# Optimization experiments

Measured on AMD Instinct MI355X. Metric: run time of the kernel, lower is better.

## Reference

```python
import jax, jax.numpy as jnp
import numpy as np

B, N, V, C, H, W = 4, 2048, 4, 64, 32, 32
D, K, OUT, HEADS = 128, 64, 256, 4
IMG_W, IMG_H = W * 14.0, H * 14.0
EPS_NORM = 1e-12


def setup_inputs() -> dict:
    key = jax.random.key(0)
    ks = iter(jax.random.split(key, 64))
    nk = lambda: next(ks)
    rn = lambda shape, s=1.0: jax.random.normal(nk(), shape, jnp.float32) * s
    eye4 = jnp.broadcast_to(jnp.eye(4, dtype=jnp.float32), (B, V, 4, 4))
    Kbase = jnp.array([[400.0, 0.0, IMG_W / 2], [0.0, 400.0, IMG_H / 2], [0.0, 0.0, 1.0]], jnp.float32)
    inp = {
        'gaussians': rn((B, N, 14)),
        'visual_feats': rn((B * V, C, H, W)),
        'extrinsics': eye4 + rn((B, V, 4, 4), 0.1),
        'intrinsics': jnp.broadcast_to(Kbase, (B, V, 3, 3)) + rn((B, V, 3, 3), 0.5),
        'offsets': rn((B, N, 2), 0.05),
        'pg_w': rn((D, 14), 0.1), 'pg_b': jnp.zeros((D,)), 'pg_ln_g': jnp.ones((D,)), 'pg_ln_b': jnp.zeros((D,)),
        'pv_w': rn((D, C), 0.1), 'pv_b': jnp.zeros((D,)), 'pv_ln_g': jnp.ones((D,)), 'pv_ln_b': jnp.zeros((D,)),
        'attn_ipw': rn((2, 3 * D, D), 0.05), 'attn_ipb': jnp.zeros((2, 3 * D)),
        'attn_ow': rn((2, D, D), 0.05), 'attn_ob': jnp.zeros((2, D)),
        'dca_ln_g': jnp.ones((2, D)), 'dca_ln_b': jnp.zeros((2, D)),
        'gate_w': rn((D, 2 * D), 0.05), 'gate_b': jnp.zeros((D,)),
        'router_w1': rn((D, 2 * D), 0.05), 'router_b1': jnp.zeros((D,)),
        'router_ln_g': jnp.ones((D,)), 'router_ln_b': jnp.zeros((D,)),
        'router_w2': rn((3, D), 0.01), 'router_b2': jnp.array([-3.0, -3.0, 2.0], jnp.float32),
        'vlad_cent': jnp.clip(rn((3, K, D), 0.01), -2.0, 2.0),
        'vlad_cw': rn((3, K, D), 0.05), 'vlad_cb': jnp.zeros((3, K)),
        'bn_w': rn((3, OUT, K * D), 0.01), 'bn_b': jnp.zeros((3, OUT)),
        'bn_ln_g': jnp.ones((3, OUT)), 'bn_ln_b': jnp.zeros((3, OUT)),
    }
    return inp


def _ln(x, g, b, eps=1e-5):
    m = x.mean(-1, keepdims=True)
    v = ((x - m) ** 2).mean(-1, keepdims=True)
    return (x - m) * jax.lax.rsqrt(v + eps) * g + b


def _l2n(x, axis):
    return x / jnp.maximum(jnp.linalg.norm(x, axis=axis, keepdims=True), EPS_NORM)


def _bilinear(fm, grid):
    # fm: [BV,H,W,C]; grid: [BV,N,2] in [-1,1]; align_corners=False, zero padding
    x = (grid[..., 0] + 1.0) * 0.5 * W - 0.5
    y = (grid[..., 1] + 1.0) * 0.5 * H - 0.5
    x0, y0 = jnp.floor(x), jnp.floor(y)
    fmf = fm.reshape(fm.shape[0], H * W, C)
    out = jnp.zeros((fm.shape[0], grid.shape[1], C), jnp.float32)
    for xi in (x0, x0 + 1.0):
        for yi in (y0, y0 + 1.0):
            wgt = (1.0 - jnp.abs(x - xi)) * (1.0 - jnp.abs(y - yi))
            valid = (xi >= 0) & (xi < W) & (yi >= 0) & (yi < H)
            idx = (jnp.clip(yi, 0, H - 1) * W + jnp.clip(xi, 0, W - 1)).astype(jnp.int32)
            v = jnp.take_along_axis(fmf, idx[..., None], axis=1)
            out = out + v * (wgt * valid.astype(jnp.float32))[..., None]
    return out


def _mha(q, k, v, ipw, ipb, ow, ob):
    Wq, Wk, Wv = jnp.split(ipw, 3, axis=0)
    bq, bk, bv = jnp.split(ipb, 3)
    dh = D // HEADS
    sh = lambda x, Wt, b: (x @ Wt.T + b).reshape(x.shape[0], x.shape[1], HEADS, dh)
    qh, kh, vh = sh(q, Wq, bq), sh(k, Wk, bk), sh(v, Wv, bv)
    att = jax.nn.softmax(jnp.einsum('bqhd,bkhd->bhqk', qh, kh) * (1.0 / np.sqrt(dh)), axis=-1)
    o = jnp.einsum('bhqk,bkhd->bqhd', att, vh).reshape(q.shape[0], q.shape[1], D)
    return o @ ow.T + ob


def _netvlad(x, cent, cw, cb):
    xn = _l2n(x, 2)                                   # [B,N,D]
    a = jax.nn.softmax(xn @ cw.T + cb, axis=-1)       # [B,N,K]
    # sum_n a[bnk]*(x[bnd]-c[kd]) without materializing [B,N,K,D]
    vlad = jnp.einsum('bnk,bnd->bkd', a, xn) - a.sum(1)[..., None] * cent
    vlad = _l2n(vlad, 2).reshape(x.shape[0], -1)
    return _l2n(vlad, 1)


def reference(gaussians, visual_feats, extrinsics, intrinsics, offsets,
              pg_w, pg_b, pg_ln_g, pg_ln_b, pv_w, pv_b, pv_ln_g, pv_ln_b,
              attn_ipw, attn_ipb, attn_ow, attn_ob, dca_ln_g, dca_ln_b,
              gate_w, gate_b, router_w1, router_b1, router_ln_g, router_ln_b,
              router_w2, router_b2, vlad_cent, vlad_cw, vlad_cb,
              bn_w, bn_b, bn_ln_g, bn_ln_b):
    # ---- DynamicProjectionLayer (vectorized over views) ----
    ph = jnp.concatenate([gaussians[:, :, :3], jnp.ones((B, N, 1), jnp.float32)], axis=2)
    cam = jnp.einsum('bvij,bnj->bvni', extrinsics, ph)          # [B,V,N,4]
    p2h = jnp.einsum('bvij,bvnj->bvni', intrinsics, cam[..., :3])
    depth = jnp.maximum(p2h[..., 2:3], 1e-6)
    p2 = p2h[..., :2] / depth
    grid = 2.0 * p2 / jnp.array([IMG_W, IMG_H], jnp.float32) - 1.0 + offsets[:, None]
    fm = visual_feats.reshape(B, V, C, H, W).transpose(0, 1, 3, 4, 2).reshape(B * V, H, W, C)
    sampled = _bilinear(fm, grid.reshape(B * V, N, 2)).reshape(B, V, N, C)
    valid = ((depth[..., 0] > 0.1) & (grid[..., 0] >= -1) & (grid[..., 0] <= 1)
             & (grid[..., 1] >= -1) & (grid[..., 1] <= 1)).astype(jnp.float32)[..., None]
    vfeat = (sampled * valid).sum(1) / (valid.sum(1) + 1e-8)     # [B,N,C]
    # ---- GaussianEncoder ----
    g_emb = jax.nn.relu(_ln(gaussians @ pg_w.T + pg_b, pg_ln_g, pg_ln_b))
    v_emb = jax.nn.relu(_ln(vfeat @ pv_w.T + pv_b, pv_ln_g, pv_ln_b))
    f_g2v = _ln(g_emb + _mha(g_emb, v_emb, v_emb, attn_ipw[0], attn_ipb[0], attn_ow[0], attn_ob[0]),
                dca_ln_g[0], dca_ln_b[0])
    f_v2g = _ln(v_emb + _mha(v_emb, g_emb, g_emb, attn_ipw[1], attn_ipb[1], attn_ow[1], attn_ob[1]),
                dca_ln_g[1], dca_ln_b[1])
    gate = jax.nn.sigmoid(jnp.concatenate([f_g2v, f_v2g], -1) @ gate_w.T + gate_b)
    fused = f_g2v * gate + f_v2g * (1.0 - gate)
    ri = jnp.concatenate([g_emb.mean(1), v_emb.mean(1)], -1)
    rw = jax.nn.softmax(jax.nn.relu(_ln(ri @ router_w1.T + router_b1, router_ln_g, router_ln_b))
                        @ router_w2.T + router_b2, axis=-1)
    descs = []
    for i, feat in enumerate((g_emb, v_emb, fused)):
        d = _netvlad(feat, vlad_cent[i], vlad_cw[i], vlad_cb[i])
        d = _ln(d @ bn_w[i].T + bn_b[i], bn_ln_g[i], bn_ln_b[i])
        descs.append(_l2n(d, 1))
    final = rw[:, 0:1] * descs[0] + rw[:, 1:2] * descs[1] + rw[:, 2:3] * descs[2]
    return _l2n(final, 1), rw
```

## Files before the change

kernel.cpp:

```cpp
#include <hip/hip_runtime.h>
#include <math.h>

typedef float f32x4 __attribute__((ext_vector_type(4)));
typedef short s16x8 __attribute__((ext_vector_type(8)));

#define DEV static __device__ __forceinline__

DEV float wsum(float v){
  #pragma unroll
  for(int m=1;m<64;m<<=1) v += __shfl_xor(v,m);
  return v;
}
template<int NW>
DEV float bsum(float v, float* s){
  v = wsum(v);
  int w = threadIdx.x>>6;
  if((threadIdx.x&63)==0) s[w]=v;
  __syncthreads();
  float r = 0.f;
  #pragma unroll
  for(int i=0;i<NW;++i) r += s[i];
  __syncthreads();
  return r;
}
DEV float xexp2(float x){
#if __has_builtin(__builtin_amdgcn_exp2f)
  return __builtin_amdgcn_exp2f(x);
#else
  return exp2f(x);
#endif
}
DEV unsigned pkbf(float lo, float hi){
  unsigned r;
  asm("v_cvt_pk_bf16_f32 %0, %1, %2" : "=v"(r) : "v"(lo), "v"(hi));
  return r;
}
DEV unsigned short bf16c(float v){ return (unsigned short)(pkbf(v, 0.f) & 0xffffu); }
DEV float ubf_lo(unsigned u){ unsigned b=(u&0xffffu)<<16; return __builtin_bit_cast(float,b); }
DEV float ubf_hi(unsigned u){ unsigned b=(u>>16)<<16;    return __builtin_bit_cast(float,b); }
union FR { unsigned u[4]; s16x8 v; uint4 q; };

DEV f32x4 MF(s16x8 a, s16x8 b, f32x4 c){
  return __builtin_amdgcn_mfma_f32_16x16x32_bf16(a, b, c, 0,0,0);
}

DEV void gl_lds16(const void* g, void* l){
  __builtin_amdgcn_global_load_lds(
    (const __attribute__((address_space(1))) void*)g,
    (__attribute__((address_space(3))) void*)l, 16, 0, 0);
}

__global__ __launch_bounds__(256) void k_proj(const float* __restrict__ gs, const float* __restrict__ vf,
                       const float* __restrict__ E, const float* __restrict__ Kin,
                       const float* __restrict__ off, float* __restrict__ vfeat){
  int bn = blockIdx.x*4 + (threadIdx.x>>6); int b = bn>>11; int c = threadIdx.x&63;
  const float* g = gs + (size_t)bn*14;
  float px = g[0], py = g[1], pz = g[2];
  float ox = off[bn*2+0], oy = off[bn*2+1];
  float acc = 0.f, vsum = 0.f;
  for(int v=0; v<4; ++v){
    const float* e = E + ((b*4+v)*16);
    float cx = e[0]*px + e[1]*py + e[2]*pz + e[3];
    float cy = e[4]*px + e[5]*py + e[6]*pz + e[7];
    float cz = e[8]*px + e[9]*py + e[10]*pz + e[11];
    const float* kk = Kin + ((b*4+v)*9);
    float ux = kk[0]*cx + kk[1]*cy + kk[2]*cz;
    float uy = kk[3]*cx + kk[4]*cy + kk[5]*cz;
    float uz = kk[6]*cx + kk[7]*cy + kk[8]*cz;
    float dep = fmaxf(uz, 1e-6f);
    float gx = 2.f*(ux/dep)*(1.f/448.f) - 1.f + ox;
    float gy = 2.f*(uy/dep)*(1.f/448.f) - 1.f + oy;
    float valid = (uz > 0.1f && gx >= -1.f && gx <= 1.f && gy >= -1.f && gy <= 1.f) ? 1.f : 0.f;
    float x = (gx+1.f)*16.f - 0.5f;
    float y = (gy+1.f)*16.f - 0.5f;
    float x0 = floorf(x), y0 = floorf(y);
    const float* fbase = vf + (size_t)((b*4+v)*64 + c)*1024;
    float sv = 0.f;
    #pragma unroll
    for(int t=0;t<4;++t){
      float xi = x0 + (float)(t&1), yi = y0 + (float)(t>>1);
      float wgt = (1.f - fabsf(x-xi))*(1.f - fabsf(y-yi));
      bool vt = (xi>=0.f && xi<32.f && yi>=0.f && yi<32.f);
      int xc = (int)fminf(fmaxf(xi,0.f),31.f);
      int yc = (int)fminf(fmaxf(yi,0.f),31.f);
      float smp = fbase[yc*32+xc];
      sv += vt ? wgt*smp : 0.f;
    }
    acc += valid * sv;
    vsum += valid;
  }
  vfeat[(size_t)bn*64 + c] = acc / (vsum + 1e-8f);
}

__global__ void k_embed(const float* __restrict__ gs, const float* __restrict__ vfeat,
   const float* __restrict__ pg_w, const float* __restrict__ pg_b,
   const float* __restrict__ pg_g, const float* __restrict__ pg_bb,
   const float* __restrict__ pv_w, const float* __restrict__ pv_b,
   const float* __restrict__ pv_g, const float* __restrict__ pv_bb,
   float* __restrict__ gemb, float* __restrict__ vemb,
   unsigned short* __restrict__ gembb, unsigned short* __restrict__ vembb){
  __shared__ float xs[64]; __shared__ float gsr[14]; __shared__ float red[2];
  int row = blockIdx.x; int d = threadIdx.x;
  if(d<14) gsr[d] = gs[(size_t)row*14+d];
  if(d<64) xs[d] = vfeat[(size_t)row*64+d];
  __syncthreads();
  float a = pg_b[d];
  #pragma unroll
  for(int j=0;j<14;++j) a += gsr[j]*pg_w[d*14+j];
  float mu = bsum<2>(a, red)*(1.f/128.f);
  float df = a-mu;
  float var = bsum<2>(df*df, red)*(1.f/128.f);
  float y = fmaxf(df*rsqrtf(var+1e-5f)*pg_g[d] + pg_bb[d], 0.f);
  gemb[(size_t)row*128+d] = y;
  gembb[(size_t)row*128+d] = bf16c(y);
  float av = pv_b[d];
  #pragma unroll
  for(int j=0;j<64;++j) av += xs[j]*pv_w[d*64+j];
  mu = bsum<2>(av, red)*(1.f/128.f);
  df = av-mu;
  var = bsum<2>(df*df, red)*(1.f/128.f);
  y = fmaxf(df*rsqrtf(var+1e-5f)*pv_g[d] + pv_bb[d], 0.f);
  vemb[(size_t)row*128+d] = y;
  vembb[(size_t)row*128+d] = bf16c(y);
}

__global__ void k_wprep(const float* __restrict__ ipw, const float* __restrict__ ow,
                        const float* __restrict__ gw, const float* __restrict__ cw,
                        unsigned short* __restrict__ WB){
  int i = blockIdx.x*256 + threadIdx.x;
  if(i >= 188416) return;
  float v;
  if(i < 98304)       v = ipw[i];
  else if(i < 131072) v = ow[i-98304];
  else if(i < 163840) v = gw[i-131072];
  else                v = cw[i-163840];
  WB[i] = bf16c(v);
}

__global__ __launch_bounds__(256) void k_qkv(const unsigned short* __restrict__ GEb,
    const unsigned short* __restrict__ VEb, const unsigned short* __restrict__ WB,
    const float* __restrict__ ipb, unsigned* __restrict__ QKVu, float qsc){
  int mt = blockIdx.x, y = blockIdx.y;
  int m = y/6, j6 = y%6, kind = j6>>1, n0 = (j6&1)*64;
  const unsigned short* A = (kind==0) ? (m?VEb:GEb) : (m?GEb:VEb);
  const unsigned short* W = WB + m*49152 + kind*16384;
  const float* bias = ipb + m*384 + kind*128;
  unsigned* outb = QKVu + (size_t)m*1572864 + (size_t)kind*524288;
  float scale = (kind==0)? qsc : 1.f;
  int m0 = mt*64;
  int wid=threadIdx.x>>6, lane=threadIdx.x&63, lr=lane&15, lg=lane>>4;
  const unsigned short* ap = A + (size_t)(m0+wid*16+lr)*128 + lg*8;
  f32x4 acc[4] = {{0,0,0,0},{0,0,0,0},{0,0,0,0},{0,0,0,0}};
  #pragma unroll
  for(int ks=0; ks<128; ks+=32){
    FR af; af.v = *(const s16x8*)(ap + ks);
    #pragma unroll
    for(int nt=0; nt<4; ++nt){
      FR bf; bf.v = *(const s16x8*)(W + (size_t)(n0+nt*16+lr)*128 + ks + lg*8);
      acc[nt] = MF(af.v, bf.v, acc[nt]);
    }
  }
  __shared__ float xs[64][65];
  #pragma unroll
  for(int nt=0; nt<4; ++nt){
    float bv = bias[n0+nt*16+lr];
    #pragma unroll
    for(int r=0;r<4;++r) xs[wid*16+lg*4+r][nt*16+lr] = (acc[nt][r]+bv)*scale;
  }
  __syncthreads();
  if(kind<2){
    int i = threadIdx.x>>2, s = threadIdx.x&3;
    int gr = m0 + i, b = gr>>11, nn = gr&2047;
    int j0 = n0 + s*16, h = j0>>5, d0 = j0&31;
    unsigned w[8];
    #pragma unroll
    for(int p=0;p<8;++p) w[p] = pkbf(xs[i][s*16+2*p], xs[i][s*16+2*p+1]);
    unsigned* dst = outb + ((size_t)(b*4+h)*2048+nn)*16 + (d0>>1);
    uint4 u0; u0.x=w[0];u0.y=w[1];u0.z=w[2];u0.w=w[3];
    uint4 u1; u1.x=w[4];u1.y=w[5];u1.z=w[6];u1.w=w[7];
    *(uint4*)dst = u0; *(uint4*)(dst+4) = u1;
  } else {
    int c = threadIdx.x>>2, rs = threadIdx.x&3;
    int j = n0 + c, h = j>>5, d = j&31;
    int b = m0>>11, nn0 = m0&2047;
    unsigned w[8];
    #pragma unroll
    for(int p=0;p<8;++p) w[p] = pkbf(xs[rs*16+2*p][c], xs[rs*16+2*p+1][c]);
    unsigned* dst = outb + (size_t)(b*4+h)*32768 + (size_t)d*1024 + ((nn0+rs*16)>>1);
    uint4 u0; u0.x=w[0];u0.y=w[1];u0.z=w[2];u0.w=w[3];
    uint4 u1; u1.x=w[4];u1.y=w[5];u1.z=w[6];u1.w=w[7];
    *(uint4*)dst = u0; *(uint4*)(dst+4) = u1;
  }
}

__global__ __launch_bounds__(256) void k_flash(const unsigned short* __restrict__ QKV,
    unsigned* __restrict__ OPARTw, float* __restrict__ LSUM){
  int qt = blockIdx.x, h = blockIdx.y, z = blockIdx.z;
  int mb = z&7, split = z>>3;
  int m = mb>>2, b = mb&3;
  const unsigned short* base = QKV + (size_t)m*3145728;
  const unsigned short* qp = base + (size_t)(b*4+h)*65536;
  const unsigned short* kp = qp + 1048576;
  const unsigned short* vp = qp + 2097152;
  int tid=threadIdx.x, wid=tid>>6, lane=tid&63, lr=lane&15, lg=lane>>4;
  __shared__ unsigned short KT[2][2048];
  __shared__ unsigned short VT[2][2048];
  __shared__ unsigned Ps[4][16][33];
  int q0 = qt*64 + wid*16;
  int kbase = split*1024;
  FR qf; qf.v = *(const s16x8*)(qp + (size_t)(q0+lr)*32 + lg*8);
  const f32x4 zz = {0.f,0.f,0.f,0.f};
  f32x4 o0g = zz, o1g = zz;
  float lrun = 0.f;
  unsigned* prow = &Ps[wid][lr][0];
  int kr = wid*16 + (lane>>2);
  int kscol = (((lane&3)<<3) ^ (((lane>>3)&3)<<3));
  const unsigned short* ksrc0 = kp + (size_t)(kbase + kr)*32 + kscol;
  int vrow = wid*8 + (lane>>3);
  int vscol = 8*((lane&7) ^ (lane>>3));
  const unsigned short* vsrc0 = vp + (size_t)vrow*2048 + kbase + vscol;
  int kkey = ((lr>>1)&3)<<3;
  int ko = lr*32 + ((lg*8) ^ kkey);
  int sw = (lr&7)*8;
  int vo0 = lr*64 + ((lg*8) ^ sw);
  int vo2 = lr*64 + ((32+lg*8) ^ sw);
  gl_lds16(ksrc0, &KT[0][wid*512]);
  gl_lds16(vsrc0, &VT[0][wid*512]);
  __syncthreads();
  int buf = 0;
  for(int t=0; t<16; ++t){
    int tn = (t+1)&15;
    gl_lds16(ksrc0 + (size_t)tn*2048, &KT[buf^1][wid*512]);
    gl_lds16(vsrc0 + tn*64,           &VT[buf^1][wid*512]);
    const unsigned short* Ktb = &KT[buf][0];
    const unsigned short* Vtb = &VT[buf][0];
    FR k0,k1,k2,k3;
    k0.v = *(const s16x8*)(Ktb + ko);
    k1.v = *(const s16x8*)(Ktb +  512 + ko);
    k2.v = *(const s16x8*)(Ktb + 1024 + ko);
    k3.v = *(const s16x8*)(Ktb + 1536 + ko);
    f32x4 s0 = MF(k0.v, qf.v, zz);
    f32x4 s1 = MF(k1.v, qf.v, zz);
    f32x4 s2 = MF(k2.v, qf.v, zz);
    f32x4 s3 = MF(k3.v, qf.v, zz);
    float p0[4],p1[4],p2[4],p3[4]; float ps=0.f;
    #pragma unroll
    for(int r=0;r<4;++r){
      p0[r]=xexp2(s0[r]); p1[r]=xexp2(s1[r]);
      p2[r]=xexp2(s2[r]); p3[r]=xexp2(s3[r]);
      ps += p0[r]+p1[r]+p2[r]+p3[r];
    }
    lrun += ps;
    asm volatile("" ::: "memory");
    prow[   lg*2+0]=pkbf(p0[0],p0[1]); prow[   lg*2+1]=pkbf(p0[2],p0[3]);
    prow[ 8+lg*2+0]=pkbf(p1[0],p1[1]); prow[ 8+lg*2+1]=pkbf(p1[2],p1[3]);
    prow[16+lg*2+0]=pkbf(p2[0],p2[1]); prow[16+lg*2+1]=pkbf(p2[2],p2[3]);
    prow[24+lg*2+0]=pkbf(p3[0],p3[1]); prow[24+lg*2+1]=pkbf(p3[2],p3[3]);
    asm volatile("" ::: "memory");
    FR pf0, pf1;
    #pragma unroll
    for(int i=0;i<4;++i){ pf0.u[i]=prow[lg*4+i]; pf1.u[i]=prow[16+lg*4+i]; }
    FR v0,v1,v2,v3;
    v0.v = *(const s16x8*)(Vtb + vo0);
    v1.v = *(const s16x8*)(Vtb + 1024 + vo0);
    v2.v = *(const s16x8*)(Vtb + vo2);
    v3.v = *(const s16x8*)(Vtb + 1024 + vo2);
    o0g = MF(v0.v, pf0.v, o0g);
    o1g = MF(v1.v, pf0.v, o1g);
    o0g = MF(v2.v, pf1.v, o0g);
    o1g = MF(v3.v, pf1.v, o1g);
    __syncthreads();
    buf ^= 1;
  }
  lrun += __shfl_xor(lrun,16); lrun += __shfl_xor(lrun,32);
  unsigned w00=pkbf(o0g[0],o0g[1]), w01=pkbf(o0g[2],o0g[3]);
  unsigned w10=pkbf(o1g[0],o1g[1]), w11=pkbf(o1g[2],o1g[3]);
  unsigned* op = OPARTw + ((size_t)(split*2+m)*8192 + (size_t)(b*2048+q0+lr))*64 + h*16 + lg*2;
  op[0]=w00; op[1]=w01; op[8]=w10; op[9]=w11;
  if(lg==0) LSUM[((size_t)(split*2+m)*16 + b*4+h)*2048 + q0+lr] = lrun;
}

__global__ __launch_bounds__(256) void k_oproj(const unsigned* __restrict__ OPARTw,
    const float* __restrict__ LSUM,
    const unsigned short* __restrict__ WB, const float* __restrict__ ob,
    const float* __restrict__ GE, const float* __restrict__ VE,
    const float* __restrict__ dg, const float* __restrict__ db,
    float* __restrict__ CC, unsigned short* __restrict__ CCb){
  int mt = blockIdx.x, m = blockIdx.y;
  int m0 = mt*64;
  const unsigned short* W = WB + 98304 + m*16384;
  const float* bias = ob + m*128;
  const float* R = m ? VE : GE;
  const float* gamma = dg + m*128;
  const float* beta  = db + m*128;
  int wid=threadIdx.x>>6, lane=threadIdx.x&63, lr=lane&15, lg=lane>>4;
  int gr = m0 + wid*16 + lr;
  int b2 = gr>>11, nn = gr&2047;
  float invh[4];
  #pragma unroll
  for(int h=0;h<4;++h){
    float l0 = LSUM[((size_t)(m*16) + b2*4+h)*2048 + nn];
    float l1 = LSUM[((size_t)((2+m)*16) + b2*4+h)*2048 + nn];
    invh[h] = 1.f/(l0+l1);
  }
  const unsigned* a0 = OPARTw + ((size_t)m*8192 + gr)*64 + lg*4;
  const unsigned* a1 = OPARTw + ((size_t)(2+m)*8192 + gr)*64 + lg*4;
  f32x4 acc[8] = {};
  #pragma unroll
  for(int ks=0; ks<4; ++ks){
    uint4 u0 = *(const uint4*)(a0 + ks*16);
    uint4 u1 = *(const uint4*)(a1 + ks*16);
    float sc = invh[ks];
    FR af;
    af.u[0] = pkbf((ubf_lo(u0.x)+ubf_lo(u1.x))*sc, (ubf_hi(u0.x)+ubf_hi(u1.x))*sc);
    af.u[1] = pkbf((ubf_lo(u0.y)+ubf_lo(u1.y))*sc, (ubf_hi(u0.y)+ubf_hi(u1.y))*sc);
    af.u[2] = pkbf((ubf_lo(u0.z)+ubf_lo(u1.z))*sc, (ubf_hi(u0.z)+ubf_hi(u1.z))*sc);
    af.u[3] = pkbf((ubf_lo(u0.w)+ubf_lo(u1.w))*sc, (ubf_hi(u0.w)+ubf_hi(u1.w))*sc);
    #pragma unroll
    for(int nt=0; nt<8; ++nt){
      FR bf; bf.v = *(const s16x8*)(W + (size_t)(nt*16+lr)*128 + ks*32 + lg*8);
      acc[nt] = MF(af.v, bf.v, acc[nt]);
    }
  }
  __shared__ float xs[64][129];
  __shared__ float mus[64], rss[64];
  #pragma unroll
  for(int nt=0; nt<8; ++nt){
    float bv = bias[nt*16+lr];
    #pragma unroll
    for(int r=0;r<4;++r){
      int row = wid*16+lg*4+r;
      xs[row][nt*16+lr] = acc[nt][r] + bv + R[(size_t)(m0+row)*128 + nt*16+lr];
    }
  }
  __syncthreads();
  if(threadIdx.x < 64){
    int row = threadIdx.x;
    float s=0.f, s2=0.f;
    #pragma unroll 8
    for(int c=0;c<128;++c){ float x = xs[row][c]; s += x; s2 += x*x; }
    float mu = s*(1.f/128.f);
    float var = fmaxf(s2*(1.f/128.f) - mu*mu, 0.f);
    mus[row] = mu; rss[row] = rsqrtf(var + 1e-5f);
  }
  __syncthreads();
  int row = threadIdx.x>>2, cs = (threadIdx.x&3)*32;
  float mu = mus[row], rs = rss[row];
  size_t obase = (size_t)(m0+row)*256 + m*128;
  #pragma unroll 8
  for(int c=cs;c<cs+32;++c){
    float y = (xs[row][c]-mu)*rs*gamma[c] + beta[c];
    CC [obase + c] = y;
    CCb[obase + c] = bf16c(y);
  }
}

__global__ __launch_bounds__(256) void k_gatef(const unsigned short* __restrict__ CCb,
    const unsigned short* __restrict__ WB, const float* __restrict__ gate_b,
    const float* __restrict__ CC, float* __restrict__ FU){
  int mt = blockIdx.x, nh = blockIdx.y;
  int m0 = mt*64, c0 = nh*64;
  const unsigned short* W = WB + 131072;
  int wid=threadIdx.x>>6, lane=threadIdx.x&63, lr=lane&15, lg=lane>>4;
  const unsigned short* ap = CCb + (size_t)(m0+wid*16+lr)*256 + lg*8;
  f32x4 acc[4] = {};
  #pragma unroll
  for(int ks=0; ks<256; ks+=32){
    FR af; af.v = *(const s16x8*)(ap + ks);
    #pragma unroll
    for(int nt=0; nt<4; ++nt){
      FR bf; bf.v = *(const s16x8*)(W + (size_t)(c0+nt*16+lr)*256 + ks + lg*8);
      acc[nt] = MF(af.v, bf.v, acc[nt]);
    }
  }
  #pragma unroll
  for(int nt=0; nt<4; ++nt){
    int col = c0 + nt*16+lr;
    float bv = gate_b[col];
    #pragma unroll
    for(int r=0;r<4;++r){
      int row = m0 + wid*16+lg*4+r;
      float gv = 1.f/(1.f+__expf(-(acc[nt][r]+bv)));
      FU[(size_t)row*128 + col] = CC[(size_t)row*256 + col]*gv
                                + CC[(size_t)row*256 + 128 + col]*(1.f-gv);
    }
  }
}

__global__ __launch_bounds__(256) void k_rpart(const float* __restrict__ gemb, const float* __restrict__ vemb,
                        float* __restrict__ part){
  int blk = blockIdx.x;
  int b = blk>>7, ch = blk&127, t = threadIdx.x;
  const float* src = (t<128)? gemb : vemb;
  int d = t&127;
  float s=0.f;
  int n0 = ch*16;
  for(int n=0;n<16;++n) s += src[((size_t)(b*2048+n0+n))*128 + d];
  part[(size_t)blk*256 + t] = s;
}
__global__ void k_router(const float* __restrict__ part, const float* __restrict__ w1,
     const float* __restrict__ b1, const float* __restrict__ lg, const float* __restrict__ lb,
     const float* __restrict__ w2, const float* __restrict__ b2,
     float* __restrict__ rw, float* __restrict__ outrw){
  __shared__ float ri[256]; __shared__ float red[2];
  int b = blockIdx.x, t = threadIdx.x;
  for(int j=t; j<256; j+=128){
    float s=0.f;
    for(int c=0;c<128;++c) s += part[(size_t)(b*128+c)*256 + j];
    ri[j] = s*(1.f/2048.f);
  }
  __syncthreads();
  float a = b1[t];
  for(int j=0;j<256;++j) a += ri[j]*w1[t*256+j];
  float mu = bsum<2>(a,red)*(1.f/128.f);
  float df = a-mu;
  float var = bsum<2>(df*df,red)*(1.f/128.f);
  float hv = fmaxf(df*rsqrtf(var+1e-5f)*lg[t]+lb[t], 0.f);
  float l0 = bsum<2>(hv*w2[t],red);
  float l1 = bsum<2>(hv*w2[128+t],red);
  float l2 = bsum<2>(hv*w2[256+t],red);
  if(t==0){
    l0+=b2[0]; l1+=b2[1]; l2+=b2[2];
    float mx = fmaxf(l0,fmaxf(l1,l2));
    float e0=__expf(l0-mx), e1=__expf(l1-mx), e2=__expf(l2-mx);
    float s=e0+e1+e2;
    rw[b*3+0]=e0/s; rw[b*3+1]=e1/s; rw[b*3+2]=e2/s;
    outrw[b*3+0]=e0/s; outrw[b*3+1]=e1/s; outrw[b*3+2]=e2/s;
  }
}

__global__ __launch_bounds__(256) void k_vlad1(
      const float* __restrict__ GE, const float* __restrict__ VE, const float* __restrict__ FU,
      const unsigned short* __restrict__ WBcw, const float* __restrict__ cbp,
      float* __restrict__ p0, float* __restrict__ p1, float* __restrict__ p2,
      float* __restrict__ asump){
  int ch = blockIdx.x, b = blockIdx.y, z = blockIdx.z;
  const float* feat = (z==0)?GE:((z==1)?VE:FU);
  const unsigned short* cwb = WBcw + z*8192;
  const float* cb = cbp + z*64;
  float* part = (z==0)?p0:((z==1)?p1:p2);
  float* asu = asump + z*8192;
  int t = threadIdx.x;
  __shared__ unsigned xnbu[64*36];
  __shared__ unsigned short xnbT[128*72];
  __shared__ unsigned abTu[64*36];
  int nbase = b*2048 + ch*64;
  {
    int r = t>>2, q = t&3;
    const float* frow = feat + (size_t)(nbase + r)*128 + q*32;
    float v[32]; float ssq = 0.f;
    #pragma unroll
    for(int i=0;i<8;++i){
      float4 f4 = *(const float4*)(frow + i*4);
      v[i*4+0]=f4.x; v[i*4+1]=f4.y; v[i*4+2]=f4.z; v[i*4+3]=f4.w;
      ssq += f4.x*f4.x+f4.y*f4.y+f4.z*f4.z+f4.w*f4.w;
    }
    ssq += __shfl_xor(ssq,1); ssq += __shfl_xor(ssq,2);
    float inv = 1.f/fmaxf(sqrtf(ssq),1e-12f);
    #pragma unroll
    for(int i=0;i<16;++i)
      xnbu[r*36 + q*8 + i] = pkbf(v[2*i]*inv, v[2*i+1]*inv);
    #pragma unroll
    for(int j=0;j<32;++j)
      xnbT[(q*32+j)*72 + r] = bf16c(v[j]*inv);
  }
  __syncthreads();
  int w = t>>6, lane = t&63, lr = lane&15, lg = lane>>4;
  {
    f32x4 acc[4] = {};
    #pragma unroll
    for(int ks=0; ks<4; ++ks){
      FR af; af.q = *(const uint4*)&xnbu[(w*16+lr)*36 + ks*16 + lg*4];
      #pragma unroll
      for(int nt=0; nt<4; ++nt){
        FR bf; bf.v = *(const s16x8*)(cwb + (size_t)(nt*16+lr)*128 + ks*32 + lg*8);
        acc[nt] = MF(af.v, bf.v, acc[nt]);
      }
    }
    float p[4][4]; float srow[4] = {0.f,0.f,0.f,0.f};
    #pragma unroll
    for(int nt=0;nt<4;++nt){
      float cbv = cb[nt*16+lr];
      #pragma unroll
      for(int rr=0;rr<4;++rr){
        p[nt][rr] = __expf(acc[nt][rr] + cbv);
        srow[rr] += p[nt][rr];
      }
    }
    #pragma unroll
    for(int rr=0;rr<4;++rr){
      float s = srow[rr];
      s += __shfl_xor(s,1); s += __shfl_xor(s,2); s += __shfl_xor(s,4); s += __shfl_xor(s,8);
      srow[rr] = 1.f/s;
    }
    #pragma unroll
    for(int nt=0;nt<4;++nt){
      int k = nt*16+lr;
      abTu[k*36 + w*8 + lg*2 + 0] = pkbf(p[nt][0]*srow[0], p[nt][1]*srow[1]);
      abTu[k*36 + w*8 + lg*2 + 1] = pkbf(p[nt][2]*srow[2], p[nt][3]*srow[3]);
    }
  }
  __syncthreads();
  {
    f32x4 acc[8] = {};
    #pragma unroll
    for(int ns=0; ns<2; ++ns){
      FR af; af.q = *(const uint4*)&abTu[(w*16+lr)*36 + ns*16 + lg*4];
      #pragma unroll
      for(int nt=0; nt<8; ++nt){
        FR bf; bf.v = *(const s16x8*)&xnbT[(nt*16+lr)*72 + ns*32 + lg*8];
        acc[nt] = MF(af.v, bf.v, acc[nt]);
      }
    }
    size_t pb = ((size_t)(b*32+ch)*64);
    #pragma unroll
    for(int nt=0; nt<8; ++nt){
      #pragma unroll
      for(int rr=0; rr<4; ++rr){
        int k = w*16+lg*4+rr;
        part[(pb + k)*128 + nt*16+lr] = acc[nt][rr];
      }
    }
  }
  if(t<64){
    float s = 0.f;
    #pragma unroll
    for(int i=0;i<32;++i){
      unsigned u = abTu[t*36+i];
      s += ubf_lo(u) + ubf_hi(u);
    }
    asu[((size_t)(b*32+ch))*64 + t] = s;
  }
}

__global__ void k_vagg2(
      const float* __restrict__ p0, const float* __restrict__ p1, const float* __restrict__ p2,
      const float* __restrict__ asump, const float* __restrict__ cent, float* __restrict__ vlad3){
  int k = blockIdx.x, b = blockIdx.y, z = blockIdx.z;
  const float* part = (z==0)?p0:((z==1)?p1:p2);
  const float* asu = asump + z*8192;
  const float* centp = cent + (size_t)z*8192;
  float* vlad = vlad3 + z*32768;
  int t = threadIdx.x;
  __shared__ float red[2];
  float v = 0.f;
  const float* pp = part + (((size_t)b*32)*64 + k)*128 + t;
  for(int ch=0; ch<32; ++ch) v += pp[(size_t)ch*8192];
  float as = 0.f;
  const float* ap = asu + (size_t)b*2048 + k;
  for(int ch=0; ch<32; ++ch) as += ap[(size_t)ch*64];
  v -= as * centp[(size_t)k*128 + t];
  float ssq = bsum<2>(v*v, red);
  float inv = 1.f/fmaxf(sqrtf(ssq),1e-12f);
  vlad[((size_t)b*64+k)*128+t] = v*inv;
}

__global__ __launch_bounds__(256) void k_desc(const float* __restrict__ vlad3,
      const float* __restrict__ bnw, const float* __restrict__ bnb, float* __restrict__ DT){
  int jg = blockIdx.x, b = blockIdx.y, z = blockIdx.z;
  const float* vlad = vlad3 + z*32768;
  const float* bw = bnw + (size_t)z*2097152;
  const float* bb = bnb + z*256;
  float* dtmp = DT + z*1024;
  int t = threadIdx.x;
  __shared__ float fl[8192]; __shared__ float red[4];
  const float4* src = (const float4*)(vlad + (size_t)b*8192);
  float4* fl4 = (float4*)fl;
  float ssq = 0.f;
  #pragma unroll
  for(int i=0;i<8;++i){
    float4 vv = src[t + i*256]; fl4[t+i*256]=vv;
    ssq += vv.x*vv.x+vv.y*vv.y+vv.z*vv.z+vv.w*vv.w;
  }
  ssq = bsum<4>(ssq, red);
  float inv = 1.f/fmaxf(sqrtf(ssq),1e-12f);
  for(int jj=0;jj<4;++jj){
    int j = jg*4 + jj;
    const float4* wp = (const float4*)(bw + (size_t)j*8192);
    float s = 0.f;
    #pragma unroll
    for(int i=0;i<8;++i){
      int f = t + i*256;
      float4 w4 = wp[f]; float4 x4 = fl4[f];
      s += w4.x*x4.x+w4.y*x4.y+w4.z*x4.z+w4.w*x4.w;
    }
    s = bsum<4>(s, red);
    if(t==0) dtmp[(size_t)b*256 + j] = s*inv + bb[j];
  }
}

__global__ void k_final(const float* __restrict__ dtmp, const float* __restrict__ lg,
      const float* __restrict__ lb, const float* __restrict__ rw, float* __restrict__ outp){
  __shared__ float red[4];
  int b = blockIdx.x, t = threadIdx.x;
  float acc = 0.f;
  for(int i=0;i<3;++i){
    float x = dtmp[(size_t)(i*4+b)*256 + t];
    float mu = bsum<4>(x,red)*(1.f/256.f);
    float df = x-mu;
    float var = bsum<4>(df*df,red)*(1.f/256.f);
    float y = df*rsqrtf(var+1e-5f)*lg[i*256+t]+lb[i*256+t];
    float n2 = bsum<4>(y*y,red);
    y = y / fmaxf(sqrtf(n2),1e-12f);
    acc += rw[b*3+i]*y;
  }
  float n2 = bsum<4>(acc*acc,red);
  outp[(size_t)b*256+t] = acc/fmaxf(sqrtf(n2),1e-12f);
}

extern "C" void kernel_launch(void* const* d_in, const int* in_sizes, int n_in,
                              void* d_out, int out_size, void* d_ws, size_t ws_size,
                              hipStream_t stream){
  const float* gaussians=(const float*)d_in[0];
  const float* visual=(const float*)d_in[1];
  const float* extr=(const float*)d_in[2];
  const float* intr=(const float*)d_in[3];
  const float* offs=(const float*)d_in[4];
  const float* pg_w=(const float*)d_in[5];
  const float* pg_b=(const float*)d_in[6];
  const float* pg_g=(const float*)d_in[7];
  const float* pg_bb=(const float*)d_in[8];
  const float* pv_w=(const float*)d_in[9];
  const float* pv_b=(const float*)d_in[10];
  const float* pv_g=(const float*)d_in[11];
  const float* pv_bb=(const float*)d_in[12];
  const float* ipw=(const float*)d_in[13];
  const float* ipb=(const float*)d_in[14];
  const float* ow=(const float*)d_in[15];
  const float* ob=(const float*)d_in[16];
  const float* dg=(const float*)d_in[17];
  const float* db=(const float*)d_in[18];
  const float* gate_w=(const float*)d_in[19];
  const float* gate_b=(const float*)d_in[20];
  const float* rw1=(const float*)d_in[21];
  const float* rb1=(const float*)d_in[22];
  const float* rlg=(const float*)d_in[23];
  const float* rlb=(const float*)d_in[24];
  const float* rw2=(const float*)d_in[25];
  const float* rb2=(const float*)d_in[26];
  const float* cent=(const float*)d_in[27];
  const float* cw=(const float*)d_in[28];
  const float* cb=(const float*)d_in[29];
  const float* bnw=(const float*)d_in[30];
  const float* bnb=(const float*)d_in[31];
  const float* blg=(const float*)d_in[32];
  const float* blb=(const float*)d_in[33];
  float* outp=(float*)d_out;
  float* ws=(float*)d_ws;

  float* VF  = ws + 1048576;
  float* GE  = ws + 1572864;
  float* VE  = ws + 2621440;
  unsigned short* GEb = (unsigned short*)(ws + 3670016);
  unsigned short* VEb = (unsigned short*)(ws + 4194304);
  unsigned* QKVu = (unsigned*)(ws + 4718592);
  float* CC  = ws + 4718592;
  unsigned short* CCb = (unsigned short*)(ws + 6815744);
  unsigned* OPARTw = (unsigned*)(ws + 7864320);
  float* FU  = ws + 8912896;
  unsigned short* WB = (unsigned short*)(ws + 9961472);
  float* DT  = ws + 10072064;
  float* RW  = ws + 10075136;
  float* VLAD3 = ws + 10075152;
  float* PART2 = ws + 10173456;
  float* ASUMP3 = ws + 11222032;
  float* LSUM  = ws + 11246608;
  float* RP    = ws + 11246608;
  float* PART0 = ws + 3670016;
  float* PART1 = ws + 7864320;
  const unsigned short* QKVh = (const unsigned short*)QKVu;

  k_proj<<<2048,256,0,stream>>>(gaussians, visual, extr, intr, offs, VF);
  k_embed<<<8192,128,0,stream>>>(gaussians, VF, pg_w,pg_b,pg_g,pg_bb,
                                 pv_w,pv_b,pv_g,pv_bb, GE, VE, GEb, VEb);
  k_rpart<<<512,256,0,stream>>>(GE, VE, RP);
  k_router<<<4,128,0,stream>>>(RP, rw1,rb1,rlg,rlb,rw2,rb2, RW, outp+1024);
  k_wprep<<<736,256,0,stream>>>(ipw, ow, gate_w, cw, WB);

  const float qsc = 1.4426950408889634f * 0.17677669529663687f;
  k_qkv<<<dim3(128,12),256,0,stream>>>(GEb, VEb, WB, ipb, QKVu, qsc);
  k_flash<<<dim3(32,4,16),256,0,stream>>>(QKVh, OPARTw, LSUM);
  k_oproj<<<dim3(128,2),256,0,stream>>>(OPARTw, LSUM, WB, ob, GE, VE, dg, db, CC, CCb);
  k_gatef<<<dim3(128,2),256,0,stream>>>(CCb, WB, gate_b, CC, FU);
  k_vlad1<<<dim3(32,4,3),256,0,stream>>>(GE, VE, FU, WB+163840, cb,
                                         PART0, PART1, PART2, ASUMP3);
  k_vagg2<<<dim3(64,4,3),128,0,stream>>>(PART0,PART1,PART2, ASUMP3, cent, VLAD3);
  k_desc<<<dim3(64,4,3),256,0,stream>>>(VLAD3, bnw, bnb, DT);
  k_final<<<4,256,0,stream>>>(DT, blg, blb, RW, outp);
}
```

Before: 199.1 us.

## Reuse bottleneck weights across batches with split-K partial sums in desc kernel

The descriptor GEMV now loads the VLAD vectors of all four batches into registers for one K slice, so each bottleneck weight row is read once rather than once per batch. K is split into eight chunks whose partial sums go to a workspace buffer. The final kernel reduces those partials and also computes the global VLAD L2 norm, which moved out of the descriptor kernel. This cuts weight traffic at the cost of higher register use and a small extra reduction step.

Measured after the change: 213.7 us. +7.3%, slower.

```diff
diff --git a/kernel.cpp b/kernel.cpp
--- a/kernel.cpp
+++ b/kernel.cpp
@@ -556,46 +556,61 @@
 }
 
 __global__ __launch_bounds__(256) void k_desc(const float* __restrict__ vlad3,
-      const float* __restrict__ bnw, const float* __restrict__ bnb, float* __restrict__ DT){
-  int jg = blockIdx.x, b = blockIdx.y, z = blockIdx.z;
-  const float* vlad = vlad3 + z*32768;
-  const float* bw = bnw + (size_t)z*2097152;
-  const float* bb = bnb + z*256;
-  float* dtmp = DT + z*1024;
-  int t = threadIdx.x;
-  __shared__ float fl[8192]; __shared__ float red[4];
-  const float4* src = (const float4*)(vlad + (size_t)b*8192);
-  float4* fl4 = (float4*)fl;
-  float ssq = 0.f;
-  #pragma unroll
-  for(int i=0;i<8;++i){
-    float4 vv = src[t + i*256]; fl4[t+i*256]=vv;
-    ssq += vv.x*vv.x+vv.y*vv.y+vv.z*vv.z+vv.w*vv.w;
-  }
-  ssq = bsum<4>(ssq, red);
-  float inv = 1.f/fmaxf(sqrtf(ssq),1e-12f);
-  for(int jj=0;jj<4;++jj){
-    int j = jg*4 + jj;
-    const float4* wp = (const float4*)(bw + (size_t)j*8192);
-    float s = 0.f;
-    #pragma unroll
-    for(int i=0;i<8;++i){
-      int f = t + i*256;
-      float4 w4 = wp[f]; float4 x4 = fl4[f];
-      s += w4.x*x4.x+w4.y*x4.y+w4.z*x4.z+w4.w*x4.w;
-    }
-    s = bsum<4>(s, red);
-    if(t==0) dtmp[(size_t)b*256 + j] = s*inv + bb[j];
-  }
-}
-
-__global__ void k_final(const float* __restrict__ dtmp, const float* __restrict__ lg,
+      const float* __restrict__ bnw, float* __restrict__ PARTD){
+  int jg = blockIdx.x, ks = blockIdx.y, z = blockIdx.z;
+  int t = threadIdx.x, j2 = t>>6, lane = t&63;
+  const float* vb = vlad3 + z*32768 + ks*1024;
+  float vreg[4][16];
+  #pragma unroll
+  for(int b=0;b<4;++b)
+    #pragma unroll
+    for(int i=0;i<16;++i) vreg[b][i] = vb[b*8192 + i*64 + lane];
+  int j = jg*4 + j2;
+  const float* wrow = bnw + (size_t)z*2097152 + (size_t)j*8192 + ks*1024;
+  float acc0=0.f, acc1=0.f, acc2=0.f, acc3=0.f;
+  #pragma unroll
+  for(int i=0;i<16;++i){
+    float w = wrow[i*64+lane];
+    acc0 += w*vreg[0][i];
+    acc1 += w*vreg[1][i];
+    acc2 += w*vreg[2][i];
+    acc3 += w*vreg[3][i];
+  }
+  #pragma unroll
+  for(int m=1;m<64;m<<=1){
+    acc0 += __shfl_xor(acc0,m); acc1 += __shfl_xor(acc1,m);
+    acc2 += __shfl_xor(acc2,m); acc3 += __shfl_xor(acc3,m);
+  }
+  if(lane==0){
+    float* pd = PARTD + (((size_t)z*256 + j)*4)*8 + ks;
+    pd[0]  = acc0;
+    pd[8]  = acc1;
+    pd[16] = acc2;
+    pd[24] = acc3;
+  }
+}
+
+__global__ void k_final(const float* __restrict__ PARTD, const float* __restrict__ vlad3,
+      const float* __restrict__ bnb, const float* __restrict__ lg,
       const float* __restrict__ lb, const float* __restrict__ rw, float* __restrict__ outp){
   __shared__ float red[4];
   int b = blockIdx.x, t = threadIdx.x;
+  float inv3[3];
+  #pragma unroll
+  for(int z=0;z<3;++z){
+    const float* vp = vlad3 + z*32768 + b*8192;
+    float ss = 0.f;
+    for(int i=t;i<8192;i+=256){ float v = vp[i]; ss += v*v; }
+    ss = bsum<4>(ss, red);
+    inv3[z] = 1.f/fmaxf(sqrtf(ss),1e-12f);
+  }
   float acc = 0.f;
   for(int i=0;i<3;++i){
-    float x = dtmp[(size_t)(i*4+b)*256 + t];
+    const float* pd = PARTD + (((size_t)i*256 + t)*4 + b)*8;
+    float s = 0.f;
+    #pragma unroll
+    for(int ks=0;ks<8;++ks) s += pd[ks];
+    float x = s*inv3[i] + bnb[i*256+t];
     float mu = bsum<4>(x,red)*(1.f/256.f);
     float df = x-mu;
     float var = bsum<4>(df*df,red)*(1.f/256.f);
@@ -659,13 +674,13 @@
   unsigned* OPARTw = (unsigned*)(ws + 7864320);
   float* FU  = ws + 8912896;
   unsigned short* WB = (unsigned short*)(ws + 9961472);
-  float* DT  = ws + 10072064;
-  float* RW  = ws + 10075136;
-  float* VLAD3 = ws + 10075152;
-  float* PART2 = ws + 10173456;
-  float* ASUMP3 = ws + 11222032;
-  float* LSUM  = ws + 11246608;
-  float* RP    = ws + 11246608;
+  float* PARTD = ws + 10072064;
+  float* RW  = ws + 10096640;
+  float* VLAD3 = ws + 10096656;
+  float* PART2 = ws + 10194960;
+  float* ASUMP3 = ws + 11243536;
+  float* LSUM  = ws + 11268112;
+  float* RP    = ws + 11268112;
   float* PART0 = ws + 3670016;
   float* PART1 = ws + 7864320;
   const unsigned short* QKVh = (const unsigned short*)QKVu;
@@ -685,6 +700,6 @@
   k_vlad1<<<dim3(32,4,3),256,0,stream>>>(GE, VE, FU, WB+163840, cb,
                                          PART0, PART1, PART2, ASUMP3);
   k_vagg2<<<dim3(64,4,3),128,0,stream>>>(PART0,PART1,PART2, ASUMP3, cent, VLAD3);
-  k_desc<<<dim3(64,4,3),256,0,stream>>>(VLAD3, bnw, bnb, DT);
-  k_final<<<4,256,0,stream>>>(DT, blg, blb, RW, outp);
-}
+  k_desc<<<dim3(64,8,3),256,0,stream>>>(VLAD3, bnw, PARTD);
+  k_final<<<4,256,0,stream>>>(PARTD, VLAD3, bnb, blg, blb, RW, outp);
+}
```
